# Performance work log

Measured on AMD Instinct MI355X. Metric: run time of the kernel, lower is better.

## Reference

```python
import jax, jax.numpy as jnp
import numpy as np

N_EMBD = 768
HEAD_SIZE = 64
B, T = 8, 4096


def setup_inputs() -> dict:
    key = jax.random.key(0)
    ks = jax.random.split(key, 7)
    s = 0.02  # small init scale for weights
    return {
        "x": jax.random.normal(ks[0], (B, T, N_EMBD), dtype=jnp.float32),
        "Wq": jax.random.normal(ks[1], (N_EMBD, HEAD_SIZE), dtype=jnp.float32) * s,
        "bq": jax.random.normal(ks[2], (HEAD_SIZE,), dtype=jnp.float32) * s,
        "Wk": jax.random.normal(ks[3], (N_EMBD, HEAD_SIZE), dtype=jnp.float32) * s,
        "bk": jax.random.normal(ks[4], (HEAD_SIZE,), dtype=jnp.float32) * s,
        "Wv": jax.random.normal(ks[5], (N_EMBD, HEAD_SIZE), dtype=jnp.float32) * s,
        "bv": jax.random.normal(ks[6], (HEAD_SIZE,), dtype=jnp.float32) * s,
    }


def reference(x, Wq, bq, Wk, bk, Wv, bv):
    # x: [B, T, C]; note: scale uses C = n_embd (input dim), per the original code.
    C = x.shape[-1]
    scale = jnp.asarray(C, x.dtype) ** -0.5
    q = x @ Wq + bq  # [B, T, H]
    k = x @ Wk + bk  # [B, T, H]
    v = x @ Wv + bv  # [B, T, H]
    wei = jnp.einsum("bqh,bkh->bqk", q, k) * scale  # [B, T, T]
    att = jax.nn.softmax(wei, axis=-1)
    # dropout p=0.0 (eval mode) -> identity
    out = jnp.einsum("bqk,bkh->bqh", att, v)  # [B, T, H]
    return out
```

## Files before the change

### kernel.cpp

```cpp
#include <hip/hip_runtime.h>
#include <stdint.h>

#define T_SEQ 4096
#define CEMB 768
#define HS 64

typedef __attribute__((ext_vector_type(8))) short bf16x8;
typedef __attribute__((ext_vector_type(16))) float f32x16;

__device__ __forceinline__ short bfru(float f) {
    uint32_t u = __builtin_bit_cast(uint32_t, f);
    return (short)((u + 0x8000u) >> 16);
}
__device__ __forceinline__ uint32_t pack2(float a, float b) {
    return (uint32_t)(uint16_t)bfru(a) | ((uint32_t)(uint16_t)bfru(b) << 16);
}

#define QSCALE (0.036084391824351615f * 1.4426950408889634f)

__global__ __launch_bounds__(256) void prep_wt(const float* __restrict__ Wq,
                                               const float* __restrict__ Wk,
                                               const float* __restrict__ Wv,
                                               short* __restrict__ wtf) {
    const int p = blockIdx.x;
    const int ct = p / 48, kq = p % 48;
    const int tid = threadIdx.x;
    const int lane = tid & 63, jp = tid >> 6;
    const int l31 = lane & 31, lhi = lane >> 5;
    const int k = kq * 16 + lhi * 8 + jp * 2;
    const int nn = ct * 32 + l31;
    const float* W = nn < 64 ? Wq : (nn < 128 ? Wk : Wv);
    const int col = nn & 63;
    uint32_t lo = (uint16_t)bfru(W[k * 64 + col]);
    uint32_t hi = (uint16_t)bfru(W[(k + 1) * 64 + col]);
    *(uint32_t*)&wtf[(p * 64 + lane) * 8 + jp * 2] = lo | (hi << 16);
}

__global__ __launch_bounds__(256, 2) void qkv_proj(const float* __restrict__ x,
        const float* __restrict__ bq, const float* __restrict__ bk, const float* __restrict__ bv,
        const short* __restrict__ wtf,
        short* __restrict__ qo, short* __restrict__ ko, short* __restrict__ vto) {
    __shared__ short S[64 * 72];
    __shared__ short Vtr[2][64 * 40];

    const int tid  = threadIdx.x;
    const int wave = tid >> 6, lane = tid & 63;
    const int l31  = lane & 31, lhi = lane >> 5;
    const int rg = wave & 1, cb = wave >> 1;
    const int rowbase = blockIdx.x * 64;

    f32x16 acc[3];
    #pragma unroll
    for (int c = 0; c < 3; ++c) {
        const int nn = (cb * 3 + c) * 32 + l31;
        const float bb = nn < 64 ? bq[nn] : (nn < 128 ? bk[nn - 64] : bv[nn - 128]);
        #pragma unroll
        for (int r = 0; r < 16; ++r) acc[c][r] = bb;
    }

    const int g = tid >> 4, j16 = tid & 15;
    float4 t[4];
    #pragma unroll
    for (int i = 0; i < 4; ++i)
        t[i] = *(const float4*)(x + (long)(rowbase + i * 16 + g) * CEMB + j16 * 4);

    for (int kt = 0; kt < 12; ++kt) {
        __syncthreads();
        #pragma unroll
        for (int i = 0; i < 4; ++i) {
            uint32_t* dst = (uint32_t*)&S[(i * 16 + g) * 72 + j16 * 4];
            dst[0] = pack2(t[i].x, t[i].y);
            dst[1] = pack2(t[i].z, t[i].w);
        }
        __syncthreads();
        if (kt < 11) {
            #pragma unroll
            for (int i = 0; i < 4; ++i)
                t[i] = *(const float4*)(x + (long)(rowbase + i * 16 + g) * CEMB + (kt + 1) * 64 + j16 * 4);
        }
        #pragma unroll
        for (int kc = 0; kc < 4; ++kc) {
            bf16x8 af = *(const bf16x8*)&S[(rg * 32 + l31) * 72 + kc * 16 + lhi * 8];
            #pragma unroll
            for (int c = 0; c < 3; ++c) {
                bf16x8 wf = *(const bf16x8*)&wtf[((cb * 3 + c) * 48 + kt * 4 + kc) * 512 + lane * 8];
                acc[c] = __builtin_amdgcn_mfma_f32_32x32x16_bf16(af, wf, acc[c], 0, 0, 0);
            }
        }
    }

    const int row0 = rowbase + rg * 32;
    #pragma unroll
    for (int c = 0; c < 3; ++c) {
        const int ct = cb * 3 + c;
        if (ct < 2) {
            #pragma unroll
            for (int r = 0; r < 16; ++r) {
                const int row = (r & 3) + 8 * (r >> 2) + 4 * lhi;
                qo[(long)(row0 + row) * HS + ct * 32 + l31] = bfru(acc[c][r] * QSCALE);
            }
        } else if (ct < 4) {
            #pragma unroll
            for (int r = 0; r < 16; ++r) {
                const int row = (r & 3) + 8 * (r >> 2) + 4 * lhi;
                ko[(long)(row0 + row) * HS + (ct - 2) * 32 + l31] = bfru(acc[c][r]);
            }
        } else {
            const int vcol = (ct - 4) * 32 + l31;
            #pragma unroll
            for (int quad = 0; quad < 4; ++quad) {
                uint32_t lo = pack2(acc[c][quad * 4 + 0], acc[c][quad * 4 + 1]);
                uint32_t hi = pack2(acc[c][quad * 4 + 2], acc[c][quad * 4 + 3]);
                uint32_t* dst = (uint32_t*)&Vtr[rg][vcol * 40 + quad * 8 + lhi * 4];
                dst[0] = lo; dst[1] = hi;
            }
        }
    }
    if (cb == 1) {
        const int b = row0 >> 12, t0 = row0 & 4095;
        short* dst = vto + ((long)b * HS + lane) * T_SEQ + t0;
        #pragma unroll
        for (int i = 0; i < 4; ++i)
            *(bf16x8*)(dst + i * 8) = *(const bf16x8*)&Vtr[rg][lane * 40 + i * 8];
    }
}

__global__ __launch_bounds__(256, 2) void attn(const short* __restrict__ qm,
        const short* __restrict__ km, const short* __restrict__ vtm,
        float* __restrict__ Op, float* __restrict__ lp, const int ks,
        float* __restrict__ outdirect) {
    const int tid  = threadIdx.x;
    const int wave = tid >> 6, lane = tid & 63;
    const int l31  = lane & 31, lhi = lane >> 5;
    const int idx  = blockIdx.x;
    const int b = idx & 7, s = (idx >> 3) % ks, qt = idx / (8 * ks);
    const int slab = T_SEQ / ks, nkt = slab / 64;
    const int qrow0 = qt * 256 + wave * 64;

    const short* qb = qm + ((long)b * T_SEQ + qrow0) * HS;
    const short* kb = km + ((long)b * T_SEQ + s * slab) * HS;
    const short* vb = vtm + (long)b * HS * T_SEQ + s * slab;

    bf16x8 qf[2][4];
    #pragma unroll
    for (int q = 0; q < 2; ++q)
        #pragma unroll
        for (int kc = 0; kc < 4; ++kc)
            qf[q][kc] = *(const bf16x8*)&qb[(q * 32 + l31) * HS + kc * 16 + lhi * 8];

    f32x16 oacc[2][2] = {};
    float lsum[2] = {0.f, 0.f};

    for (int kt = 0; kt < nkt; ++kt) {
        const int k0 = kt * 64;
        bf16x8 kf[2][4];
        #pragma unroll
        for (int m = 0; m < 2; ++m)
            #pragma unroll
            for (int kc = 0; kc < 4; ++kc)
                kf[m][kc] = *(const bf16x8*)&kb[(k0 + m * 32 + l31) * HS + kc * 16 + lhi * 8];
        bf16x8 vf[2][4];
        #pragma unroll
        for (int ht = 0; ht < 2; ++ht)
            #pragma unroll
            for (int kv = 0; kv < 4; ++kv)
                vf[ht][kv] = *(const bf16x8*)&vb[(ht * 32 + l31) * T_SEQ + k0 + kv * 16 + lhi * 8];

        #pragma unroll
        for (int m = 0; m < 2; ++m) {
            #pragma unroll
            for (int q = 0; q < 2; ++q) {
                f32x16 z = {};
                #pragma unroll
                for (int kc = 0; kc < 4; ++kc)
                    z = __builtin_amdgcn_mfma_f32_32x32x16_bf16(kf[m][kc], qf[q][kc], z, 0, 0, 0);

                uint32_t w[8];
                #pragma unroll
                for (int qd = 0; qd < 4; ++qd) {
                    uint32_t u0 = (__builtin_bit_cast(uint32_t, __builtin_amdgcn_exp2f(z[qd * 4 + 0])) + 0x8000u) & 0xFFFF0000u;
                    uint32_t u1 = (__builtin_bit_cast(uint32_t, __builtin_amdgcn_exp2f(z[qd * 4 + 1])) + 0x8000u) & 0xFFFF0000u;
                    uint32_t u2 = (__builtin_bit_cast(uint32_t, __builtin_amdgcn_exp2f(z[qd * 4 + 2])) + 0x8000u) & 0xFFFF0000u;
                    uint32_t u3 = (__builtin_bit_cast(uint32_t, __builtin_amdgcn_exp2f(z[qd * 4 + 3])) + 0x8000u) & 0xFFFF0000u;
                    lsum[q] += (__builtin_bit_cast(float, u0) + __builtin_bit_cast(float, u1))
                             + (__builtin_bit_cast(float, u2) + __builtin_bit_cast(float, u3));
                    w[qd * 2 + 0] = (u0 >> 16) | u1;
                    w[qd * 2 + 1] = (u2 >> 16) | u3;
                }
                const bool hi = (lhi != 0);
                uint32_t sa0 = hi ? w[0] : w[2], sa1 = hi ? w[1] : w[3];
                uint32_t sb0 = hi ? w[4] : w[6], sb1 = hi ? w[5] : w[7];
                uint32_t ra0 = (uint32_t)__shfl_xor((int)sa0, 32, 64);
                uint32_t ra1 = (uint32_t)__shfl_xor((int)sa1, 32, 64);
                uint32_t rb0 = (uint32_t)__shfl_xor((int)sb0, 32, 64);
                uint32_t rb1 = (uint32_t)__shfl_xor((int)sb1, 32, 64);
                uint32_t pf0[4], pf1[4];
                pf0[0] = hi ? ra0 : w[0];  pf0[1] = hi ? ra1 : w[1];
                pf0[2] = hi ? w[2] : ra0;  pf0[3] = hi ? w[3] : ra1;
                pf1[0] = hi ? rb0 : w[4];  pf1[1] = hi ? rb1 : w[5];
                pf1[2] = hi ? w[6] : rb0;  pf1[3] = hi ? w[7] : rb1;
                bf16x8 p0 = *(const bf16x8*)pf0, p1 = *(const bf16x8*)pf1;

                #pragma unroll
                for (int ht = 0; ht < 2; ++ht) {
                    oacc[ht][q] = __builtin_amdgcn_mfma_f32_32x32x16_bf16(vf[ht][m * 2 + 0], p0, oacc[ht][q], 0, 0, 0);
                    oacc[ht][q] = __builtin_amdgcn_mfma_f32_32x32x16_bf16(vf[ht][m * 2 + 1], p1, oacc[ht][q], 0, 0, 0);
                }
            }
        }
    }

    lsum[0] += __shfl_xor(lsum[0], 32, 64);
    lsum[1] += __shfl_xor(lsum[1], 32, 64);

    const long rowg = (long)b * T_SEQ + qrow0;
    if (outdirect) {
        float* ob = outdirect + rowg * HS;
        #pragma unroll
        for (int q = 0; q < 2; ++q) {
            const float inv = 1.0f / lsum[q];
            #pragma unroll
            for (int ht = 0; ht < 2; ++ht)
                #pragma unroll
                for (int r = 0; r < 16; ++r) {
                    const int h = (r & 3) + 8 * (r >> 2) + 4 * lhi + 32 * ht;
                    ob[(long)(q * 32 + l31) * HS + h] = oacc[ht][q][r] * inv;
                }
        }
    } else {
        float* op = Op + ((long)s * 32768 + rowg) * HS;
        #pragma unroll
        for (int q = 0; q < 2; ++q) {
            #pragma unroll
            for (int ht = 0; ht < 2; ++ht)
                #pragma unroll
                for (int r = 0; r < 16; ++r) {
                    const int h = (r & 3) + 8 * (r >> 2) + 4 * lhi + 32 * ht;
                    op[(long)(q * 32 + l31) * HS + h] = oacc[ht][q][r];
                }
            if (lhi == 0)
                lp[(long)s * 32768 + rowg + q * 32 + l31] = lsum[q];
        }
    }
}

__global__ __launch_bounds__(256) void combine(const float4* __restrict__ Op,
        const float* __restrict__ lp, float4* __restrict__ out, const int ks) {
    const int idx = blockIdx.x * 256 + threadIdx.x;
    const int row = idx >> 4, h4 = idx & 15;
    float ox = 0.f, oy = 0.f, oz = 0.f, ow = 0.f, l = 0.f;
    for (int s = 0; s < ks; ++s) {
        float4 t = Op[(long)(s * 32768 + row) * 16 + h4];
        ox += t.x; oy += t.y; oz += t.z; ow += t.w;
        l += lp[s * 32768 + row];
    }
    const float inv = 1.0f / l;
    float4 o; o.x = ox * inv; o.y = oy * inv; o.z = oz * inv; o.w = ow * inv;
    out[(long)row * 16 + h4] = o;
}

extern "C" void kernel_launch(void* const* d_in, const int* in_sizes, int n_in,
                              void* d_out, int out_size, void* d_ws, size_t ws_size,
                              hipStream_t stream) {
    const float* x  = (const float*)d_in[0];
    const float* Wq = (const float*)d_in[1];
    const float* bq = (const float*)d_in[2];
    const float* Wk = (const float*)d_in[3];
    const float* bk = (const float*)d_in[4];
    const float* Wv = (const float*)d_in[5];
    const float* bv = (const float*)d_in[6];

    char* ws = (char*)d_ws;
    short* qo  = (short*)(ws);
    short* ko  = (short*)(ws + (4u << 20));
    short* vto = (short*)(ws + (8u << 20));
    short* wtf = (short*)(ws + (12u << 20));
    const size_t opOff = 12582912u + 294912u;
    float* Op = (float*)(ws + opOff);

    const size_t per_s = 8388608u + 131072u;
    int ks = (ws_size >= opOff + 4 * per_s) ? 4
           : (ws_size >= opOff + 2 * per_s) ? 2 : 1;
    float* lp = (float*)(ws + opOff + (size_t)ks * 8388608u);

    prep_wt<<<288, 256, 0, stream>>>(Wq, Wk, Wv, wtf);
    qkv_proj<<<512, 256, 0, stream>>>(x, bq, bk, bv, wtf, qo, ko, vto);
    attn<<<8 * ks * 16, 256, 0, stream>>>(qo, ko, vto, Op, lp, ks,
                                          ks == 1 ? (float*)d_out : nullptr);
    if (ks > 1)
        combine<<<2048, 256, 0, stream>>>((const float4*)Op, lp, (float4*)d_out, ks);
}
```

Measured before the change: 247.2 us.

## Stage K/V tiles in swizzled LDS, vectorize output stores, allow ks=8 split

Each K/V tile is now loaded cooperatively once per block into XOR-swizzled shared memory, and waves read their MFMA fragments from there. Previously every wave fetched the full tile from global memory itself. The exp-to-bf16 conversion switches from round-to-nearest to truncation, and output writes become float4 stores. The KV split can rise to 8 when the workspace allows it. These changes add two block barriers per tile and more partial-output traffic for the combine step, and the truncation slightly shifts numerics.

```diff
diff --git a/kernel.cpp b/kernel.cpp
--- a/kernel.cpp
+++ b/kernel.cpp
@@ -129,6 +129,9 @@
         const short* __restrict__ km, const short* __restrict__ vtm,
         float* __restrict__ Op, float* __restrict__ lp, const int ks,
         float* __restrict__ outdirect) {
+    __shared__ short Kt[64 * 64];
+    __shared__ short Vt[64 * 64];
+
     const int tid  = threadIdx.x;
     const int wave = tid >> 6, lane = tid & 63;
     const int l31  = lane & 31, lhi = lane >> 5;
@@ -151,37 +154,51 @@
     f32x16 oacc[2][2] = {};
     float lsum[2] = {0.f, 0.f};
 
+    const int strow = tid >> 2, stc = (tid & 3) * 16, g0 = (tid & 3) * 2;
+    const int sw0 = strow * 64 + ((g0 ^ (strow & 7)) * 8);
+    const int sw1 = strow * 64 + (((g0 + 1) ^ (strow & 7)) * 8);
+
     for (int kt = 0; kt < nkt; ++kt) {
         const int k0 = kt * 64;
-        bf16x8 kf[2][4];
-        #pragma unroll
-        for (int m = 0; m < 2; ++m)
-            #pragma unroll
-            for (int kc = 0; kc < 4; ++kc)
-                kf[m][kc] = *(const bf16x8*)&kb[(k0 + m * 32 + l31) * HS + kc * 16 + lhi * 8];
-        bf16x8 vf[2][4];
-        #pragma unroll
-        for (int ht = 0; ht < 2; ++ht)
-            #pragma unroll
-            for (int kv = 0; kv < 4; ++kv)
-                vf[ht][kv] = *(const bf16x8*)&vb[(ht * 32 + l31) * T_SEQ + k0 + kv * 16 + lhi * 8];
+        bf16x8 ka = *(const bf16x8*)&kb[(k0 + strow) * HS + stc];
+        bf16x8 kc2_ = *(const bf16x8*)&kb[(k0 + strow) * HS + stc + 8];
+        bf16x8 va = *(const bf16x8*)&vb[strow * T_SEQ + k0 + stc];
+        bf16x8 vc2_ = *(const bf16x8*)&vb[strow * T_SEQ + k0 + stc + 8];
+        *(bf16x8*)&Kt[sw0] = ka;  *(bf16x8*)&Kt[sw1] = kc2_;
+        *(bf16x8*)&Vt[sw0] = va;  *(bf16x8*)&Vt[sw1] = vc2_;
+        __syncthreads();
 
         #pragma unroll
         for (int m = 0; m < 2; ++m) {
+            bf16x8 kf[4];
+            #pragma unroll
+            for (int kc = 0; kc < 4; ++kc) {
+                const int r = m * 32 + l31, gk = kc * 2 + lhi;
+                kf[kc] = *(const bf16x8*)&Kt[r * 64 + ((gk ^ (r & 7)) * 8)];
+            }
+            bf16x8 vf[2][2];
+            #pragma unroll
+            for (int ht = 0; ht < 2; ++ht)
+                #pragma unroll
+                for (int j = 0; j < 2; ++j) {
+                    const int hr = ht * 32 + l31, gv = (m * 2 + j) * 2 + lhi;
+                    vf[ht][j] = *(const bf16x8*)&Vt[hr * 64 + ((gv ^ (hr & 7)) * 8)];
+                }
+
             #pragma unroll
             for (int q = 0; q < 2; ++q) {
                 f32x16 z = {};
                 #pragma unroll
                 for (int kc = 0; kc < 4; ++kc)
-                    z = __builtin_amdgcn_mfma_f32_32x32x16_bf16(kf[m][kc], qf[q][kc], z, 0, 0, 0);
+                    z = __builtin_amdgcn_mfma_f32_32x32x16_bf16(kf[kc], qf[q][kc], z, 0, 0, 0);
 
                 uint32_t w[8];
                 #pragma unroll
                 for (int qd = 0; qd < 4; ++qd) {
-                    uint32_t u0 = (__builtin_bit_cast(uint32_t, __builtin_amdgcn_exp2f(z[qd * 4 + 0])) + 0x8000u) & 0xFFFF0000u;
-                    uint32_t u1 = (__builtin_bit_cast(uint32_t, __builtin_amdgcn_exp2f(z[qd * 4 + 1])) + 0x8000u) & 0xFFFF0000u;
-                    uint32_t u2 = (__builtin_bit_cast(uint32_t, __builtin_amdgcn_exp2f(z[qd * 4 + 2])) + 0x8000u) & 0xFFFF0000u;
-                    uint32_t u3 = (__builtin_bit_cast(uint32_t, __builtin_amdgcn_exp2f(z[qd * 4 + 3])) + 0x8000u) & 0xFFFF0000u;
+                    uint32_t u0 = __builtin_bit_cast(uint32_t, __builtin_amdgcn_exp2f(z[qd * 4 + 0])) & 0xFFFF0000u;
+                    uint32_t u1 = __builtin_bit_cast(uint32_t, __builtin_amdgcn_exp2f(z[qd * 4 + 1])) & 0xFFFF0000u;
+                    uint32_t u2 = __builtin_bit_cast(uint32_t, __builtin_amdgcn_exp2f(z[qd * 4 + 2])) & 0xFFFF0000u;
+                    uint32_t u3 = __builtin_bit_cast(uint32_t, __builtin_amdgcn_exp2f(z[qd * 4 + 3])) & 0xFFFF0000u;
                     lsum[q] += (__builtin_bit_cast(float, u0) + __builtin_bit_cast(float, u1))
                              + (__builtin_bit_cast(float, u2) + __builtin_bit_cast(float, u3));
                     w[qd * 2 + 0] = (u0 >> 16) | u1;
@@ -203,11 +220,12 @@
 
                 #pragma unroll
                 for (int ht = 0; ht < 2; ++ht) {
-                    oacc[ht][q] = __builtin_amdgcn_mfma_f32_32x32x16_bf16(vf[ht][m * 2 + 0], p0, oacc[ht][q], 0, 0, 0);
-                    oacc[ht][q] = __builtin_amdgcn_mfma_f32_32x32x16_bf16(vf[ht][m * 2 + 1], p1, oacc[ht][q], 0, 0, 0);
-                }
-            }
-        }
+                    oacc[ht][q] = __builtin_amdgcn_mfma_f32_32x32x16_bf16(vf[ht][0], p0, oacc[ht][q], 0, 0, 0);
+                    oacc[ht][q] = __builtin_amdgcn_mfma_f32_32x32x16_bf16(vf[ht][1], p1, oacc[ht][q], 0, 0, 0);
+                }
+            }
+        }
+        __syncthreads();
     }
 
     lsum[0] += __shfl_xor(lsum[0], 32, 64);
@@ -222,9 +240,11 @@
             #pragma unroll
             for (int ht = 0; ht < 2; ++ht)
                 #pragma unroll
-                for (int r = 0; r < 16; ++r) {
-                    const int h = (r & 3) + 8 * (r >> 2) + 4 * lhi + 32 * ht;
-                    ob[(long)(q * 32 + l31) * HS + h] = oacc[ht][q][r] * inv;
+                for (int rq = 0; rq < 4; ++rq) {
+                    float4 o;
+                    o.x = oacc[ht][q][rq * 4 + 0] * inv; o.y = oacc[ht][q][rq * 4 + 1] * inv;
+                    o.z = oacc[ht][q][rq * 4 + 2] * inv; o.w = oacc[ht][q][rq * 4 + 3] * inv;
+                    *(float4*)&ob[(long)(q * 32 + l31) * HS + rq * 8 + 4 * lhi + 32 * ht] = o;
                 }
         }
     } else {
@@ -234,9 +254,11 @@
             #pragma unroll
             for (int ht = 0; ht < 2; ++ht)
                 #pragma unroll
-                for (int r = 0; r < 16; ++r) {
-                    const int h = (r & 3) + 8 * (r >> 2) + 4 * lhi + 32 * ht;
-                    op[(long)(q * 32 + l31) * HS + h] = oacc[ht][q][r];
+                for (int rq = 0; rq < 4; ++rq) {
+                    float4 o;
+                    o.x = oacc[ht][q][rq * 4 + 0]; o.y = oacc[ht][q][rq * 4 + 1];
+                    o.z = oacc[ht][q][rq * 4 + 2]; o.w = oacc[ht][q][rq * 4 + 3];
+                    *(float4*)&op[(long)(q * 32 + l31) * HS + rq * 8 + 4 * lhi + 32 * ht] = o;
                 }
             if (lhi == 0)
                 lp[(long)s * 32768 + rowg + q * 32 + l31] = lsum[q];
@@ -279,7 +301,8 @@
     float* Op = (float*)(ws + opOff);
 
     const size_t per_s = 8388608u + 131072u;
-    int ks = (ws_size >= opOff + 4 * per_s) ? 4
+    int ks = (ws_size >= opOff + 8 * per_s) ? 8
+           : (ws_size >= opOff + 4 * per_s) ? 4
            : (ws_size >= opOff + 2 * per_s) ? 2 : 1;
     float* lp = (float*)(ws + opOff + (size_t)ks * 8388608u);
 
```

New measurement: 232.2 us. -6.1%, faster.
